# Kernel tuning notes

Measured on AMD Instinct MI355X. Metric: run time of the kernel, lower is better.

Reference implementation:

```python
import jax, jax.numpy as jnp
import numpy as np

B, S, D, M = 4, 8192, 1024, 512  # batch, seq_len, dim, memory_dim (= dim // 2)
LN_EPS = 1e-5


def _layernorm(z, g, b):
    mu = jnp.mean(z, axis=-1, keepdims=True)
    var = jnp.var(z, axis=-1, keepdims=True)
    return (z - mu) * jax.lax.rsqrt(var + LN_EPS) * g + b


def setup_inputs() -> dict:
    key = jax.random.key(0)
    ks = jax.random.split(key, 16)
    s_d = 1.0 / np.sqrt(D)
    s_m = 1.0 / np.sqrt(M)
    return {
        "x": jax.random.normal(ks[0], (B, S, D), jnp.float32),
        "Wd": jax.random.normal(ks[1], (D, M), jnp.float32) * s_d,
        "bd": jnp.zeros((M,), jnp.float32),
        "Wq": jax.random.normal(ks[2], (M, M), jnp.float32) * s_m,
        "bq": jnp.zeros((M,), jnp.float32),
        "Wk": jax.random.normal(ks[3], (M, M), jnp.float32) * s_m,
        "bk": jnp.zeros((M,), jnp.float32),
        "Wv": jax.random.normal(ks[4], (M, M), jnp.float32) * s_m,
        "bv": jnp.zeros((M,), jnp.float32),
        "gq": jnp.ones((M,), jnp.float32),
        "bq_ln": jnp.zeros((M,), jnp.float32),
        "gk": jnp.ones((M,), jnp.float32),
        "bk_ln": jnp.zeros((M,), jnp.float32),
        "W1": jax.random.normal(ks[5], (M, M), jnp.float32) * s_m,  # MemoryMLP layer 1
        "W2": jax.random.normal(ks[6], (M, M), jnp.float32) * s_m,  # MemoryMLP layer 2
        "Wu": jax.random.normal(ks[7], (M, D), jnp.float32) * s_m,
        "bu": jnp.zeros((D,), jnp.float32),
        "adaptive_lr": jnp.float32(0.01),
        "forget_factor": jnp.float32(0.1),
    }


def reference(x, Wd, bd, Wq, bq, Wk, bk, Wv, bv, gq, bq_ln, gk, bk_ln,
              W1, W2, Wu, bu, adaptive_lr, forget_factor):
    # project to memory dim: [B,S,M]
    h = jnp.einsum('bsd,dm->bsm', x, Wd) + bd
    q = _layernorm(h @ Wq + bq, gq, bq_ln)
    k = _layernorm(h @ Wk + bk, gk, bk_ln)
    v = h @ Wv + bv
    # MemoryMLP prediction on keys (depth 2, gelu between)
    pred = jax.nn.gelu(k @ W1) @ W2
    # surprise (negative gradient direction of MSE store loss), lr-scaled
    u = adaptive_lr * (v - pred)                       # inputs to scan [B,S,M]
    g = jax.nn.sigmoid(forget_factor)                  # scalar retention gate
    gates = jnp.full((B, S, 1), g, dtype=x.dtype)
    # gated linear recurrence s_t = g_t * s_{t-1} + u_t  (AssocScan math)
    def combine(a, c):
        g1, u1 = a
        g2, u2 = c
        return (g1 * g2, u1 * g2 + u2)
    _, mem = jax.lax.associative_scan(combine, (gates, u), axis=1)  # [B,S,M]
    # query-gated readout, project up, residual ('mal' integration)
    retrieved = q * mem
    out = x + jnp.einsum('bsm,md->bsd', retrieved, Wu) + bu
    return out
```

## Files before the change

kernel.cpp:

```cpp
#include <hip/hip_runtime.h>
#include <hip/hip_bf16.h>
#include <cstdint>


typedef unsigned short u16;
typedef unsigned int u32;
typedef __attribute__((ext_vector_type(4))) short short4v;
typedef __attribute__((ext_vector_type(8))) short short8;
typedef __attribute__((ext_vector_type(4))) float f32x4;

#define R_ROWS 32768
#define S_LEN 8192
#define D_DIM 1024
#define M_DIM 512

__device__ __forceinline__ float bf2f(u16 u) {
  union { unsigned int i; float f; } v; v.i = ((unsigned int)u) << 16; return v.f;
}
__device__ __forceinline__ u16 f2bf(float f) {
  union { float f; unsigned int i; } v; v.f = f;
  unsigned int r = v.i + 0x7fff + ((v.i >> 16) & 1);
  return (u16)(r >> 16);
}

__global__ __launch_bounds__(256)
void prep_all(const float* __restrict__ x, u16* __restrict__ xb,
              const float* __restrict__ Wd, const float* __restrict__ Wq,
              const float* __restrict__ Wk, const float* __restrict__ Wv,
              const float* __restrict__ W1, const float* __restrict__ W2,
              const float* __restrict__ Wu, const float* __restrict__ bq,
              const float* __restrict__ bk, const float* __restrict__ bv,
              u16* __restrict__ WdT, u16* __restrict__ WqkvT,
              u16* __restrict__ W1T, u16* __restrict__ W2T,
              u16* __restrict__ WuT, float* __restrict__ bqkv) {
  __shared__ u16 tile[32][33];
  int id = blockIdx.x;
  if (id >= 2310) {
    const long i = ((long)(id - 2310) * 256 + threadIdx.x) * 8;
    const f32x4 a = *(const f32x4*)(x + i);
    const f32x4 b = *(const f32x4*)(x + i + 4);
    short8 o;
    o[0] = (short)f2bf(a[0]); o[1] = (short)f2bf(a[1]);
    o[2] = (short)f2bf(a[2]); o[3] = (short)f2bf(a[3]);
    o[4] = (short)f2bf(b[0]); o[5] = (short)f2bf(b[1]);
    o[6] = (short)f2bf(b[2]); o[7] = (short)f2bf(b[3]);
    *(short8*)(xb + i) = o;
    return;
  }
  if (id >= 2304) {
    const int i = (id - 2304) * 256 + threadIdx.x;
    bqkv[i] = (i < 512) ? bq[i] : (i < 1024) ? bk[i - 512] : bv[i - 1024];
    return;
  }
  const float* src;
  u16* dst;
  int rows, cols, bx, by;
  if (id < 512) {
    src = Wd; dst = WdT; rows = 1024; cols = 512;
    bx = id & 15; by = id >> 4;
  } else if (id < 768) {
    src = Wq; dst = WqkvT; rows = 512; cols = 512;
    id -= 512; bx = id & 15; by = id >> 4;
  } else if (id < 1024) {
    src = Wk; dst = WqkvT + 512 * 512; rows = 512; cols = 512;
    id -= 768; bx = id & 15; by = id >> 4;
  } else if (id < 1280) {
    src = Wv; dst = WqkvT + 2 * 512 * 512; rows = 512; cols = 512;
    id -= 1024; bx = id & 15; by = id >> 4;
  } else if (id < 1536) {
    src = W1; dst = W1T; rows = 512; cols = 512;
    id -= 1280; bx = id & 15; by = id >> 4;
  } else if (id < 1792) {
    src = W2; dst = W2T; rows = 512; cols = 512;
    id -= 1536; bx = id & 15; by = id >> 4;
  } else {
    src = Wu; dst = WuT; rows = 512; cols = 1024;
    id -= 1792; bx = id & 31; by = id >> 5;
  }
  const int tx = threadIdx.x & 31;
  const int ty = threadIdx.x >> 5;
  const int c = bx * 32 + tx;
#pragma unroll
  for (int i = 0; i < 32; i += 8)
    tile[ty + i][tx] = f2bf(src[(long)(by * 32 + ty + i) * cols + c]);
  __syncthreads();
  const int c2 = by * 32 + tx;
#pragma unroll
  for (int i = 0; i < 32; i += 8)
    dst[(long)(bx * 32 + ty + i) * rows + c2] = tile[tx][ty + i];
}


#define BARRIER()                          \
  __builtin_amdgcn_sched_barrier(0);       \
  __builtin_amdgcn_s_barrier();            \
  __builtin_amdgcn_sched_barrier(0)

#define RD_A(D, QM, AF)                                                     \
  _Pragma("unroll") for (int mi = 0; mi < 4; ++mi)                          \
  _Pragma("unroll") for (int kk = 0; kk < 2; ++kk)                          \
    AF[mi][kk] = *(const short8*)(smem + (D) * 65536 +                      \
        (wm * 128 + (QM) * 64 + mi * 16 + l15) * 128 +                      \
        ((kk * 64 + lg * 16) ^ xre));

#define RD_B(D, QN, BF)                                                     \
  _Pragma("unroll") for (int j = 0; j < 2; ++j)                             \
  _Pragma("unroll") for (int kk = 0; kk < 2; ++kk)                          \
    BF[j][kk] = *(const short8*)(smem + (D) * 65536 + 32768 +               \
        (wn * 64 + (QN) * 32 + j * 16 + l15) * 128 +                        \
        ((kk * 64 + lg * 16) ^ xre));

#define DO_MFMA(QM, QN, AF, BF)                                             \
  __builtin_amdgcn_s_setprio(1);                                            \
  _Pragma("unroll") for (int mi = 0; mi < 4; ++mi)                          \
  _Pragma("unroll") for (int j = 0; j < 2; ++j)                             \
  _Pragma("unroll") for (int kk = 0; kk < 2; ++kk)                          \
    acc[(QM) * 4 + mi][(QN) * 2 + j] =                                      \
        __builtin_amdgcn_mfma_f32_16x16x32_bf16(                            \
            AF[mi][kk], BF[j][kk], acc[(QM) * 4 + mi][(QN) * 2 + j], 0, 0, 0); \
  __builtin_amdgcn_s_setprio(0)

template <int EPI>
__global__ __launch_bounds__(512, 1)
void gemm8p(const u16* __restrict__ A, const u16* __restrict__ BT,
            const float* __restrict__ bias, void* __restrict__ Cv,
            const int K, const int N,
            const void* __restrict__ auxv, const float* __restrict__ sclr) {
  __shared__ __align__(16) char smem[131072];
  const int tid = threadIdx.x;
  const int lane = tid & 63;
  const int wid = tid >> 6;
  const int l15 = lane & 15;
  const int lg = lane >> 4;
  const int wm = wid >> 2;
  const int wn = wid & 3;
  const long am0 = (long)blockIdx.x * 256;
  const long bn0 = (long)blockIdx.y * 256;
  const int s_r = lane >> 3;
  const int s_c = ((lane & 7) << 3) ^ ((lane >> 3) << 3);
  const int xre = (l15 & 7) << 4;

  f32x4 acc[8][4];
#pragma unroll
  for (int i = 0; i < 8; ++i)
#pragma unroll
    for (int j = 0; j < 4; ++j) acc[i][j] = (f32x4){0.f, 0.f, 0.f, 0.f};

  const int NT = K >> 6;
  const int NITER = NT >> 1;

  auto stg = [&](int d, int arr, int half, int kt) {
    const int k0 = kt << 6;
    const u16* src = arr ? BT : A;
    const long rb0 = arr ? bn0 : am0;
    char* base = smem + d * 65536 + arr * 32768 + half * 16384;
#pragma unroll
    for (int i = 0; i < 2; ++i) {
      const int jr = (wid * 2 + i) * 8;
      const u16* g =
          src + (rb0 + half * 128 + jr + s_r) * (long)K + (k0 + s_c);
      __builtin_amdgcn_global_load_lds(
          (const __attribute__((address_space(1))) void*)g,
          (__attribute__((address_space(3))) void*)(base + jr * 128), 16, 0, 0);
    }
  };

  stg(0, 1, 0, 0); stg(0, 1, 1, 0);
  stg(0, 0, 0, 0); stg(0, 0, 1, 0);
  stg(1, 1, 0, 1); stg(1, 1, 1, 1);
  asm volatile("s_waitcnt vmcnt(4)" ::: "memory");
  BARRIER();

  short8 aF[4][2], bF0[2][2], bF1[2][2];
#pragma unroll 1
  for (int t = 0; t < NITER; ++t) {
    const int kt1 = 2 * t + 1;
    const int kt2 = (2 * t + 2 < NT) ? 2 * t + 2 : NT - 1;
    const int kt3 = (2 * t + 3 < NT) ? 2 * t + 3 : NT - 1;
    RD_A(0, 0, aF); RD_B(0, 0, bF0);
    stg(1, 0, 0, kt1);
    BARRIER();
    DO_MFMA(0, 0, aF, bF0);
    BARRIER();
    RD_B(0, 1, bF1);
    stg(1, 0, 1, kt1);
    BARRIER();
    DO_MFMA(0, 1, aF, bF1);
    BARRIER();
    RD_A(0, 1, aF);
    stg(0, 1, 0, kt2);
    BARRIER();
    DO_MFMA(1, 1, aF, bF1);
    BARRIER();
    stg(0, 1, 1, kt2);
    BARRIER();
    DO_MFMA(1, 0, aF, bF0);
    asm volatile("s_waitcnt vmcnt(4)" ::: "memory");
    BARRIER();
    RD_A(1, 0, aF); RD_B(1, 0, bF0);
    stg(0, 0, 0, kt2);
    BARRIER();
    DO_MFMA(0, 0, aF, bF0);
    BARRIER();
    RD_B(1, 1, bF1);
    stg(0, 0, 1, kt2);
    BARRIER();
    DO_MFMA(0, 1, aF, bF1);
    BARRIER();
    RD_A(1, 1, aF);
    stg(1, 1, 0, kt3);
    BARRIER();
    DO_MFMA(1, 1, aF, bF1);
    BARRIER();
    stg(1, 1, 1, kt3);
    BARRIER();
    DO_MFMA(1, 0, aF, bF0);
    asm volatile("s_waitcnt vmcnt(4)" ::: "memory");
    BARRIER();
  }

  float* Cs = (float*)smem;
  float lr = 0.f;
  if (EPI == 2) lr = *sclr;
  const int tseg = (tid & 63) * 4;
  const int trw = tid >> 6;
  u16* Cb = nullptr;
  long cb0 = bn0;
  int Nout = N;
  if constexpr (EPI != 3) {
    if constexpr (EPI == 4) {
      const long sel = bn0 >> 9;
      Cb = (u16*)Cv + sel * ((long)R_ROWS * M_DIM);
      cb0 = bn0 & 511;
      Nout = M_DIM;
    } else {
      Cb = (u16*)Cv;
    }
  }
#pragma unroll
  for (int p = 0; p < 8; ++p) {
    __syncthreads();
    if (wm == (p >> 2)) {
      const int mbase = (p & 3) * 2;
#pragma unroll
      for (int mm = 0; mm < 2; ++mm)
#pragma unroll
        for (int ni = 0; ni < 4; ++ni)
#pragma unroll
          for (int r = 0; r < 4; ++r)
            Cs[(mm * 16 + lg * 4 + r) * 260 + wn * 64 + ni * 16 + l15] =
                acc[mbase + mm][ni][r];
    }
    __syncthreads();
#pragma unroll
    for (int rb = 0; rb < 32; rb += 8) {
      const int lrow = rb + trw;
      const long row = am0 + p * 32 + lrow;
      f32x4 cv = *(const f32x4*)&Cs[lrow * 260 + tseg];
      if constexpr (EPI == 3) {
        const u16* xb = (const u16*)auxv;
        float* Of = (float*)Cv;
        const long col = bn0 + tseg;
        const u32* xp = (const u32*)(xb + row * N + col);
        const u32 x0 = xp[0], x1 = xp[1];
        const f32x4 bv = *(const f32x4*)&bias[col];
        cv[0] += bf2f((u16)(x0 & 0xffff)) + bv[0];
        cv[1] += bf2f((u16)(x0 >> 16)) + bv[1];
        cv[2] += bf2f((u16)(x1 & 0xffff)) + bv[2];
        cv[3] += bf2f((u16)(x1 >> 16)) + bv[3];
        *(f32x4*)&Of[row * N + col] = cv;
      } else {
        if constexpr (EPI == 0 || EPI == 4) {
          const f32x4 bv = *(const f32x4*)&bias[bn0 + tseg];
#pragma unroll
          for (int j = 0; j < 4; ++j) cv[j] += bv[j];
        } else if constexpr (EPI == 1) {
#pragma unroll
          for (int j = 0; j < 4; ++j) {
            const float c = cv[j];
            cv[j] = 0.5f * c *
                (1.f + tanhf(0.7978845608028654f * (c + 0.044715f * c * c * c)));
          }
        } else if constexpr (EPI == 2) {
          const u16* aux = (const u16*)auxv;
          const u32* ap = (const u32*)(aux + row * Nout + cb0 + tseg);
          const u32 a0 = ap[0], a1 = ap[1];
          cv[0] = lr * (bf2f((u16)(a0 & 0xffff)) - cv[0]);
          cv[1] = lr * (bf2f((u16)(a0 >> 16)) - cv[1]);
          cv[2] = lr * (bf2f((u16)(a1 & 0xffff)) - cv[2]);
          cv[3] = lr * (bf2f((u16)(a1 >> 16)) - cv[3]);
        }
        short4v o;
        o[0] = (short)f2bf(cv[0]);
        o[1] = (short)f2bf(cv[1]);
        o[2] = (short)f2bf(cv[2]);
        o[3] = (short)f2bf(cv[3]);
        *(short4v*)&Cb[row * Nout + cb0 + tseg] = o;
      }
    }
  }
}

__global__ __launch_bounds__(256)
void ln_k_qstat(u16* __restrict__ k, const u16* __restrict__ q,
                const float* __restrict__ gk, const float* __restrict__ bk,
                float2* __restrict__ statq) {
  const int wid = threadIdx.x >> 6, lane = threadIdx.x & 63;
  if (blockIdx.x < 8192) {
    const long job = (long)blockIdx.x * 4 + wid;
    u16* p = k + job * M_DIM + lane * 8;
    short8 zv = *(short8*)p;
    float z[8], s = 0.f, s2 = 0.f;
#pragma unroll
    for (int i = 0; i < 8; ++i) {
      z[i] = bf2f((u16)zv[i]);
      s += z[i];
      s2 += z[i] * z[i];
    }
#pragma unroll
    for (int off = 32; off >= 1; off >>= 1) {
      s += __shfl_xor(s, off);
      s2 += __shfl_xor(s2, off);
    }
    const float mu = s * (1.f / 512.f);
    const float inv = rsqrtf(s2 * (1.f / 512.f) - mu * mu + 1e-5f);
#pragma unroll
    for (int i = 0; i < 8; ++i) {
      float y = (z[i] - mu) * inv * gk[lane * 8 + i] + bk[lane * 8 + i];
      zv[i] = (short)f2bf(y);
    }
    *(short8*)p = zv;
  } else {
    const long job = (long)(blockIdx.x - 8192) * 4 + wid;
    const short8 zv = *(const short8*)(q + job * M_DIM + lane * 8);
    float s = 0.f, s2 = 0.f;
#pragma unroll
    for (int i = 0; i < 8; ++i) {
      const float z = bf2f((u16)zv[i]);
      s += z;
      s2 += z * z;
    }
#pragma unroll
    for (int off = 32; off >= 1; off >>= 1) {
      s += __shfl_xor(s, off);
      s2 += __shfl_xor(s2, off);
    }
    const float mu = s * (1.f / 512.f);
    const float inv = rsqrtf(s2 * (1.f / 512.f) - mu * mu + 1e-5f);
    if (lane == 0) statq[job] = make_float2(mu, inv);
  }
}

#define SCAN_CH 64
#define SCAN_L (S_LEN / SCAN_CH)
#define SCAN_W 64

__global__ __launch_bounds__(256)
void scan_mul(const u16* __restrict__ u, const u16* __restrict__ q,
              u16* __restrict__ retr, const float* __restrict__ ffp,
              const float2* __restrict__ statq, const float* __restrict__ gq,
              const float* __restrict__ bq_ln) {
  const int m2 = threadIdx.x;
  const int b = blockIdx.x / SCAN_CH;
  const int ch = blockIdx.x % SCAN_CH;
  const float g = 1.f / (1.f + __expf(-*ffp));
  const int c0 = 2 * m2;
  const float g0 = gq[c0], g1 = gq[c0 + 1];
  const float b0 = bq_ln[c0], b1 = bq_ln[c0 + 1];
  const long rbase = (long)b * S_LEN;
  const long base = rbase * M_DIM + c0;
  const int t0 = ch * SCAN_L;
  const int tw = (t0 >= SCAN_W) ? (t0 - SCAN_W) : 0;
  float s0 = 0.f, s1 = 0.f;
#pragma unroll 8
  for (int t = tw; t < t0; ++t) {
    const u32 w = *(const u32*)(u + base + (long)t * M_DIM);
    s0 = g * s0 + bf2f((u16)(w & 0xffff));
    s1 = g * s1 + bf2f((u16)(w >> 16));
  }
#pragma unroll 4
  for (int t = t0; t < t0 + SCAN_L; ++t) {
    const long idx = base + (long)t * M_DIM;
    const u32 w = *(const u32*)(u + idx);
    s0 = g * s0 + bf2f((u16)(w & 0xffff));
    s1 = g * s1 + bf2f((u16)(w >> 16));
    const u32 qw = *(const u32*)(q + idx);
    const float2 st = statq[rbase + t];
    const float q0 = (bf2f((u16)(qw & 0xffff)) - st.x) * st.y * g0 + b0;
    const float q1 = (bf2f((u16)(qw >> 16)) - st.x) * st.y * g1 + b1;
    const u32 o = (u32)f2bf(q0 * s0) | ((u32)f2bf(q1 * s1) << 16);
    *(u32*)(retr + idx) = o;
  }
}

extern "C" void kernel_launch(void* const* d_in, const int* in_sizes, int n_in,
                              void* d_out, int out_size, void* d_ws,
                              size_t ws_size, hipStream_t stream) {
  const float* x = (const float*)d_in[0];
  const float* Wd = (const float*)d_in[1];
  const float* bd = (const float*)d_in[2];
  const float* Wq = (const float*)d_in[3];
  const float* bq = (const float*)d_in[4];
  const float* Wk = (const float*)d_in[5];
  const float* bk = (const float*)d_in[6];
  const float* Wv = (const float*)d_in[7];
  const float* bv = (const float*)d_in[8];
  const float* gq = (const float*)d_in[9];
  const float* bq_ln = (const float*)d_in[10];
  const float* gk = (const float*)d_in[11];
  const float* bk_ln = (const float*)d_in[12];
  const float* W1 = (const float*)d_in[13];
  const float* W2 = (const float*)d_in[14];
  const float* Wu = (const float*)d_in[15];
  const float* bu = (const float*)d_in[16];
  const float* lr = (const float*)d_in[17];
  const float* ff = (const float*)d_in[18];

  char* w = (char*)d_ws;
  auto alloc = [&](size_t bytes) {
    char* p = w;
    w += (bytes + 255) & ~(size_t)255;
    return (u16*)p;
  };
  u16* WdT = alloc(512 * 1024 * 2);
  u16* WqkvT = alloc((size_t)1536 * 512 * 2);
  u16* W1T = alloc(512 * 512 * 2);
  u16* W2T = alloc(512 * 512 * 2);
  u16* WuT = alloc(1024 * 512 * 2);
  float* bqkv = (float*)alloc(1536 * 4);
  float2* statq = (float2*)alloc((size_t)R_ROWS * 8);
  const size_t act = (size_t)R_ROWS * M_DIM * 2;
  u16* xb = alloc(2 * act);
  u16* hB = alloc(act);
  u16* qB = alloc(act);
  u16* kB = alloc(act);
  u16* vB = alloc(act);
  u16* t1 = hB;
  u16* uB = kB;
  u16* retr = vB;

  dim3 tb(256);
  prep_all<<<dim3(2310 + 16384), tb, 0, stream>>>(
      x, xb, Wd, Wq, Wk, Wv, W1, W2, Wu, bq, bk, bv,
      WdT, WqkvT, W1T, W2T, WuT, bqkv);

  gemm8p<0><<<dim3(128, 2), 512, 0, stream>>>(xb, WdT, bd, hB, 1024, 512, nullptr, nullptr);
  gemm8p<4><<<dim3(128, 6), 512, 0, stream>>>(hB, WqkvT, bqkv, qB, 512, 512, nullptr, nullptr);
  ln_k_qstat<<<dim3(16384), tb, 0, stream>>>(kB, qB, gk, bk_ln, statq);
  gemm8p<1><<<dim3(128, 2), 512, 0, stream>>>(kB, W1T, nullptr, t1, 512, 512, nullptr, nullptr);
  gemm8p<2><<<dim3(128, 2), 512, 0, stream>>>(t1, W2T, nullptr, uB, 512, 512, vB, lr);
  scan_mul<<<dim3(4 * SCAN_CH), tb, 0, stream>>>(uB, qB, retr, ff, statq, gq, bq_ln);
  gemm8p<3><<<dim3(128, 4), 512, 0, stream>>>(retr, WuT, bu, d_out, 512, 1024, xb, nullptr);
}
```

Before: 322.6 us.

## Replace 256x256 pipelined GEMM with 64x512 tile, K=32 double-buffered kernel

Replaces the heavily scheduled 256x256-tile GEMM (128KB LDS, 8-phase barrier pipeline, one block per CU) with a simpler kernel that uses 64-row by 512-column tiles, K-step 32, and plain double buffering in about 72KB of LDS. Each wave computes 64x64 outputs, and launch bounds allow more blocks so that occupancy, rather than hand scheduling, hides latency. The grid grows to 512 row-blocks. Each B tile now spans the whole N=512 width, so A is read only once, but per-tile reuse of B and the MFMA-to-load ratio are lower than before. The epilogue is adapted to the 512-wide tile.

```diff
diff --git a/kernel.cpp b/kernel.cpp
--- a/kernel.cpp
+++ b/kernel.cpp
@@ -90,140 +90,82 @@
     dst[(long)(bx * 32 + ty + i) * rows + c2] = tile[tx][ty + i];
 }
 
-
-#define BARRIER()                          \
-  __builtin_amdgcn_sched_barrier(0);       \
-  __builtin_amdgcn_s_barrier();            \
-  __builtin_amdgcn_sched_barrier(0)
-
-#define RD_A(D, QM, AF)                                                     \
-  _Pragma("unroll") for (int mi = 0; mi < 4; ++mi)                          \
-  _Pragma("unroll") for (int kk = 0; kk < 2; ++kk)                          \
-    AF[mi][kk] = *(const short8*)(smem + (D) * 65536 +                      \
-        (wm * 128 + (QM) * 64 + mi * 16 + l15) * 128 +                      \
-        ((kk * 64 + lg * 16) ^ xre));
-
-#define RD_B(D, QN, BF)                                                     \
-  _Pragma("unroll") for (int j = 0; j < 2; ++j)                             \
-  _Pragma("unroll") for (int kk = 0; kk < 2; ++kk)                          \
-    BF[j][kk] = *(const short8*)(smem + (D) * 65536 + 32768 +               \
-        (wn * 64 + (QN) * 32 + j * 16 + l15) * 128 +                        \
-        ((kk * 64 + lg * 16) ^ xre));
-
-#define DO_MFMA(QM, QN, AF, BF)                                             \
-  __builtin_amdgcn_s_setprio(1);                                            \
-  _Pragma("unroll") for (int mi = 0; mi < 4; ++mi)                          \
-  _Pragma("unroll") for (int j = 0; j < 2; ++j)                             \
-  _Pragma("unroll") for (int kk = 0; kk < 2; ++kk)                          \
-    acc[(QM) * 4 + mi][(QN) * 2 + j] =                                      \
-        __builtin_amdgcn_mfma_f32_16x16x32_bf16(                            \
-            AF[mi][kk], BF[j][kk], acc[(QM) * 4 + mi][(QN) * 2 + j], 0, 0, 0); \
-  __builtin_amdgcn_s_setprio(0)
-
 template <int EPI>
-__global__ __launch_bounds__(512, 1)
-void gemm8p(const u16* __restrict__ A, const u16* __restrict__ BT,
-            const float* __restrict__ bias, void* __restrict__ Cv,
-            const int K, const int N,
-            const void* __restrict__ auxv, const float* __restrict__ sclr) {
-  __shared__ __align__(16) char smem[131072];
+__global__ __launch_bounds__(512, 4)
+void gemm_t64(const u16* __restrict__ A, const u16* __restrict__ BT,
+              const float* __restrict__ bias, void* __restrict__ Cv,
+              const int K, const int N,
+              const void* __restrict__ auxv, const float* __restrict__ sclr) {
+  __shared__ __align__(16) char smem[73728];
   const int tid = threadIdx.x;
   const int lane = tid & 63;
   const int wid = tid >> 6;
   const int l15 = lane & 15;
   const int lg = lane >> 4;
-  const int wm = wid >> 2;
-  const int wn = wid & 3;
-  const long am0 = (long)blockIdx.x * 256;
-  const long bn0 = (long)blockIdx.y * 256;
-  const int s_r = lane >> 3;
-  const int s_c = ((lane & 7) << 3) ^ ((lane >> 3) << 3);
-  const int xre = (l15 & 7) << 4;
-
-  f32x4 acc[8][4];
-#pragma unroll
-  for (int i = 0; i < 8; ++i)
+  const long am0 = (long)blockIdx.x * 64;
+  const long bn0 = (long)blockIdx.y * 512;
+  const int s_r = lane >> 2;
+  const int s_c = (((lane & 3) ^ ((lane >> 2) & 3)) << 3);
+  const int xre = (l15 & 3) << 4;
+
+  f32x4 acc[4][4];
+#pragma unroll
+  for (int i = 0; i < 4; ++i)
 #pragma unroll
     for (int j = 0; j < 4; ++j) acc[i][j] = (f32x4){0.f, 0.f, 0.f, 0.f};
 
-  const int NT = K >> 6;
-  const int NITER = NT >> 1;
-
-  auto stg = [&](int d, int arr, int half, int kt) {
-    const int k0 = kt << 6;
-    const u16* src = arr ? BT : A;
-    const long rb0 = arr ? bn0 : am0;
-    char* base = smem + d * 65536 + arr * 32768 + half * 16384;
-#pragma unroll
-    for (int i = 0; i < 2; ++i) {
-      const int jr = (wid * 2 + i) * 8;
-      const u16* g =
-          src + (rb0 + half * 128 + jr + s_r) * (long)K + (k0 + s_c);
+  const int NT = K >> 5;
+
+  auto stg = [&](int d, int kt) {
+    const int k0 = kt << 5;
+    char* bufA = smem + d * 36864;
+    char* bufB = bufA + 4096;
+    if (wid < 4) {
+      const int j = wid;
+      const u16* g = A + (am0 + j * 16 + s_r) * (long)K + (k0 + s_c);
       __builtin_amdgcn_global_load_lds(
           (const __attribute__((address_space(1))) void*)g,
-          (__attribute__((address_space(3))) void*)(base + jr * 128), 16, 0, 0);
+          (__attribute__((address_space(3))) void*)(bufA + j * 1024), 16, 0, 0);
+    }
+#pragma unroll
+    for (int i = 0; i < 4; ++i) {
+      const int j = wid * 4 + i;
+      const u16* g = BT + (bn0 + j * 16 + s_r) * (long)K + (k0 + s_c);
+      __builtin_amdgcn_global_load_lds(
+          (const __attribute__((address_space(1))) void*)g,
+          (__attribute__((address_space(3))) void*)(bufB + j * 1024), 16, 0, 0);
     }
   };
 
-  stg(0, 1, 0, 0); stg(0, 1, 1, 0);
-  stg(0, 0, 0, 0); stg(0, 0, 1, 0);
-  stg(1, 1, 0, 1); stg(1, 1, 1, 1);
-  asm volatile("s_waitcnt vmcnt(4)" ::: "memory");
-  BARRIER();
-
-  short8 aF[4][2], bF0[2][2], bF1[2][2];
+  stg(0, 0);
+  __syncthreads();
 #pragma unroll 1
-  for (int t = 0; t < NITER; ++t) {
-    const int kt1 = 2 * t + 1;
-    const int kt2 = (2 * t + 2 < NT) ? 2 * t + 2 : NT - 1;
-    const int kt3 = (2 * t + 3 < NT) ? 2 * t + 3 : NT - 1;
-    RD_A(0, 0, aF); RD_B(0, 0, bF0);
-    stg(1, 0, 0, kt1);
-    BARRIER();
-    DO_MFMA(0, 0, aF, bF0);
-    BARRIER();
-    RD_B(0, 1, bF1);
-    stg(1, 0, 1, kt1);
-    BARRIER();
-    DO_MFMA(0, 1, aF, bF1);
-    BARRIER();
-    RD_A(0, 1, aF);
-    stg(0, 1, 0, kt2);
-    BARRIER();
-    DO_MFMA(1, 1, aF, bF1);
-    BARRIER();
-    stg(0, 1, 1, kt2);
-    BARRIER();
-    DO_MFMA(1, 0, aF, bF0);
-    asm volatile("s_waitcnt vmcnt(4)" ::: "memory");
-    BARRIER();
-    RD_A(1, 0, aF); RD_B(1, 0, bF0);
-    stg(0, 0, 0, kt2);
-    BARRIER();
-    DO_MFMA(0, 0, aF, bF0);
-    BARRIER();
-    RD_B(1, 1, bF1);
-    stg(0, 0, 1, kt2);
-    BARRIER();
-    DO_MFMA(0, 1, aF, bF1);
-    BARRIER();
-    RD_A(1, 1, aF);
-    stg(1, 1, 0, kt3);
-    BARRIER();
-    DO_MFMA(1, 1, aF, bF1);
-    BARRIER();
-    stg(1, 1, 1, kt3);
-    BARRIER();
-    DO_MFMA(1, 0, aF, bF0);
-    asm volatile("s_waitcnt vmcnt(4)" ::: "memory");
-    BARRIER();
+  for (int t = 0; t < NT; ++t) {
+    if (t + 1 < NT) stg((t + 1) & 1, t + 1);
+    const char* bufA = smem + (t & 1) * 36864;
+    const char* bufB = bufA + 4096;
+    short8 aF[4], bF[4];
+#pragma unroll
+    for (int mi = 0; mi < 4; ++mi)
+      aF[mi] = *(const short8*)(bufA + (mi * 16 + l15) * 64 + ((lg << 4) ^ xre));
+#pragma unroll
+    for (int ni = 0; ni < 4; ++ni)
+      bF[ni] = *(const short8*)(bufB + (wid * 64 + ni * 16 + l15) * 64 +
+                                ((lg << 4) ^ xre));
+#pragma unroll
+    for (int mi = 0; mi < 4; ++mi)
+#pragma unroll
+      for (int ni = 0; ni < 4; ++ni)
+        acc[mi][ni] = __builtin_amdgcn_mfma_f32_16x16x32_bf16(
+            aF[mi], bF[ni], acc[mi][ni], 0, 0, 0);
+    __syncthreads();
   }
 
   float* Cs = (float*)smem;
   float lr = 0.f;
   if (EPI == 2) lr = *sclr;
-  const int tseg = (tid & 63) * 4;
-  const int trw = tid >> 6;
+  const int tseg = (tid & 127) * 4;
+  const int trw = tid >> 7;
   u16* Cb = nullptr;
   long cb0 = bn0;
   int Nout = N;
@@ -231,32 +173,30 @@
     if constexpr (EPI == 4) {
       const long sel = bn0 >> 9;
       Cb = (u16*)Cv + sel * ((long)R_ROWS * M_DIM);
-      cb0 = bn0 & 511;
+      cb0 = 0;
       Nout = M_DIM;
     } else {
       Cb = (u16*)Cv;
     }
   }
 #pragma unroll
-  for (int p = 0; p < 8; ++p) {
+  for (int p = 0; p < 2; ++p) {
+#pragma unroll
+    for (int mm = 0; mm < 2; ++mm) {
+      const int mi = p * 2 + mm;
+#pragma unroll
+      for (int ni = 0; ni < 4; ++ni)
+#pragma unroll
+        for (int r = 0; r < 4; ++r)
+          Cs[(mm * 16 + lg * 4 + r) * 516 + wid * 64 + ni * 16 + l15] =
+              acc[mi][ni][r];
+    }
     __syncthreads();
-    if (wm == (p >> 2)) {
-      const int mbase = (p & 3) * 2;
-#pragma unroll
-      for (int mm = 0; mm < 2; ++mm)
-#pragma unroll
-        for (int ni = 0; ni < 4; ++ni)
-#pragma unroll
-          for (int r = 0; r < 4; ++r)
-            Cs[(mm * 16 + lg * 4 + r) * 260 + wn * 64 + ni * 16 + l15] =
-                acc[mbase + mm][ni][r];
-    }
-    __syncthreads();
-#pragma unroll
-    for (int rb = 0; rb < 32; rb += 8) {
+#pragma unroll
+    for (int rb = 0; rb < 32; rb += 4) {
       const int lrow = rb + trw;
       const long row = am0 + p * 32 + lrow;
-      f32x4 cv = *(const f32x4*)&Cs[lrow * 260 + tseg];
+      f32x4 cv = *(const f32x4*)&Cs[lrow * 516 + tseg];
       if constexpr (EPI == 3) {
         const u16* xb = (const u16*)auxv;
         float* Of = (float*)Cv;
@@ -298,6 +238,7 @@
         *(short4v*)&Cb[row * Nout + cb0 + tseg] = o;
       }
     }
+    __syncthreads();
   }
 }
 
@@ -444,11 +385,11 @@
       x, xb, Wd, Wq, Wk, Wv, W1, W2, Wu, bq, bk, bv,
       WdT, WqkvT, W1T, W2T, WuT, bqkv);
 
-  gemm8p<0><<<dim3(128, 2), 512, 0, stream>>>(xb, WdT, bd, hB, 1024, 512, nullptr, nullptr);
-  gemm8p<4><<<dim3(128, 6), 512, 0, stream>>>(hB, WqkvT, bqkv, qB, 512, 512, nullptr, nullptr);
+  gemm_t64<0><<<dim3(512, 1), 512, 0, stream>>>(xb, WdT, bd, hB, 1024, 512, nullptr, nullptr);
+  gemm_t64<4><<<dim3(512, 3), 512, 0, stream>>>(hB, WqkvT, bqkv, qB, 512, 512, nullptr, nullptr);
   ln_k_qstat<<<dim3(16384), tb, 0, stream>>>(kB, qB, gk, bk_ln, statq);
-  gemm8p<1><<<dim3(128, 2), 512, 0, stream>>>(kB, W1T, nullptr, t1, 512, 512, nullptr, nullptr);
-  gemm8p<2><<<dim3(128, 2), 512, 0, stream>>>(t1, W2T, nullptr, uB, 512, 512, vB, lr);
+  gemm_t64<1><<<dim3(512, 1), 512, 0, stream>>>(kB, W1T, nullptr, t1, 512, 512, nullptr, nullptr);
+  gemm_t64<2><<<dim3(512, 1), 512, 0, stream>>>(t1, W2T, nullptr, uB, 512, 512, vB, lr);
   scan_mul<<<dim3(4 * SCAN_CH), tb, 0, stream>>>(uB, qB, retr, ff, statq, gq, bq_ln);
-  gemm8p<3><<<dim3(128, 4), 512, 0, stream>>>(retr, WuT, bu, d_out, 512, 1024, xb, nullptr);
-}
+  gemm_t64<3><<<dim3(512, 2), 512, 0, stream>>>(retr, WuT, bu, d_out, 512, 1024, xb, nullptr);
+}
```

Result: slower. 359.8 us (+11.5%).
